# Kernel optimization log

Hardware: AMD Instinct MI355X
Metric: run time of the kernel (lower is better)

Reference implementation:

```python
import jax, jax.numpy as jnp
import numpy as np

N = 100000   # nodes
E = 600000   # edges
D = 128      # in_dim == out_dim
ED = 6       # edge_dim
LN_EPS = 1e-5


def setup_inputs() -> dict:
    key = jax.random.key(0)
    ks = jax.random.split(key, 12)
    s = 1.0 / np.sqrt(D)
    se = 1.0 / np.sqrt(ED)
    return {
        "x": jax.random.normal(ks[0], (N, D), dtype=jnp.float32),
        "edge_index": jax.random.randint(ks[1], (2, E), 0, N, dtype=jnp.int64),
        "edge_attr": jax.random.normal(ks[2], (E, ED), dtype=jnp.float32),
        "batch": jnp.zeros((N,), dtype=jnp.int64),
        "W_e": jax.random.uniform(ks[3], (ED, D), jnp.float32, -se, se),
        "b_e": jax.random.uniform(ks[4], (D,), jnp.float32, -se, se),
        "eps": jnp.zeros((), dtype=jnp.float32),  # GINE train_eps init 0
        "W1": jax.random.uniform(ks[5], (D, D), jnp.float32, -s, s),
        "b1": jax.random.uniform(ks[6], (D,), jnp.float32, -s, s),
        "W2": jax.random.uniform(ks[7], (D, D), jnp.float32, -s, s),
        "b2": jax.random.uniform(ks[8], (D,), jnp.float32, -s, s),
        "gamma": jnp.ones((D,), dtype=jnp.float32),
        "beta": jnp.zeros((D,), dtype=jnp.float32),
    }


def reference(x, edge_index, edge_attr, batch, W_e, b_e, eps, W1, b1, W2, b2, gamma, beta):
    src, dst = edge_index[0], edge_index[1]
    # edge embedding: Linear(edge_dim -> in_dim)
    edge_emb = edge_attr @ W_e + b_e                      # [E, D]
    # GINEConv message: ReLU(x_j + edge_emb), scatter-add to target nodes
    msg = jax.nn.relu(x[src] + edge_emb)                  # [E, D]
    agg = jax.ops.segment_sum(msg, dst, num_segments=N)   # [N, D]
    h = (1.0 + eps) * x + agg                             # [N, D]
    # GINE nn: Linear -> ReLU -> Linear
    h = jax.nn.relu(h @ W1 + b1) @ W2 + b2                # [N, D]
    # LayerNorm over feature dim
    mu = jnp.mean(h, axis=-1, keepdims=True)
    var = jnp.var(h, axis=-1, keepdims=True)
    h = (h - mu) * jax.lax.rsqrt(var + LN_EPS) * gamma + beta
    # activation=True -> ReLU; dropout identity in eval mode
    return jax.nn.relu(h)
```

## Files before the change

kernel.cpp:

```cpp
#include <hip/hip_runtime.h>
#include <stdint.h>

#define NN 100000
#define EE 600000
#define DD 128

typedef _Float16 half8 __attribute__((ext_vector_type(8)));
typedef _Float16 h2 __attribute__((ext_vector_type(2)));
typedef float f32x4 __attribute__((ext_vector_type(4)));

static __device__ __forceinline__ uint32_t pack2(float a, float b) {
    h2 h; h.x = (_Float16)a; h.y = (_Float16)b;
    return __builtin_bit_cast(uint32_t, h);
}
static __device__ __forceinline__ h2 cvt22(float2 f) {
    h2 r; r.x = (_Float16)f.x; r.y = (_Float16)f.y; return r;
}
static __device__ __forceinline__ h2 bc_lo(h2 v) { h2 r; r.x = v.x; r.y = v.x; return r; }
static __device__ __forceinline__ h2 bc_hi(h2 v) { h2 r; r.x = v.y; r.y = v.y; return r; }

static __device__ __forceinline__ void edge_msg(uint32_t rY, uint32_t rZ, uint32_t rW,
                                                uint32_t xv, uint32_t bb,
                                                uint32_t w0, uint32_t w1, uint32_t w2,
                                                uint32_t w3, uint32_t w4, uint32_t w5,
                                                float wgt, float& ax, float& ay)
{
    uint32_t m;
    asm("v_pk_add_f16 %0, %1, %2" : "=v"(m) : "v"(xv), "v"(bb));
    asm("v_pk_fma_f16 %0, %1, %2, %0 op_sel:[0,0,0] op_sel_hi:[0,1,1]" : "+v"(m) : "v"(rY), "v"(w0));
    asm("v_pk_fma_f16 %0, %1, %2, %0 op_sel:[1,0,0] op_sel_hi:[1,1,1]" : "+v"(m) : "v"(rY), "v"(w1));
    asm("v_pk_fma_f16 %0, %1, %2, %0 op_sel:[0,0,0] op_sel_hi:[0,1,1]" : "+v"(m) : "v"(rZ), "v"(w2));
    asm("v_pk_fma_f16 %0, %1, %2, %0 op_sel:[1,0,0] op_sel_hi:[1,1,1]" : "+v"(m) : "v"(rZ), "v"(w3));
    asm("v_pk_fma_f16 %0, %1, %2, %0 op_sel:[0,0,0] op_sel_hi:[0,1,1]" : "+v"(m) : "v"(rW), "v"(w4));
    asm("v_pk_fma_f16 %0, %1, %2, %0 op_sel:[1,0,0] op_sel_hi:[1,1,1]" : "+v"(m) : "v"(rW), "v"(w5));
    asm("v_pk_max_f16 %0, %0, 0" : "+v"(m));
    h2 mh = __builtin_bit_cast(h2, m);
    ax = fmaf(wgt, (float)mh.x, ax);
    ay = fmaf(wgt, (float)mh.y, ay);
}

#define NB_HIST ((EE + 255) / 256)
#define NB_CONV (NN * DD / 4 / 256)
template<bool CONV>
__global__ __launch_bounds__(256)
void setup_kernel(const int* __restrict__ ei, const float* __restrict__ x,
                  const float* __restrict__ W1, const float* __restrict__ W2,
                  int* __restrict__ counts, uint32_t* __restrict__ xh,
                  _Float16* __restrict__ w1h, _Float16* __restrict__ w2h)
{
    const int nbc = CONV ? NB_CONV : 0;
    const int b = blockIdx.x, tid = threadIdx.x;
    if (b < NB_HIST) {
        int e = b * 256 + tid;
        if (e < EE) atomicAdd(&counts[ei[EE + e]], 1);
    } else if (CONV && b < NB_HIST + nbc) {
        int i = (b - NB_HIST) * 256 + tid;
        float4 v = ((const float4*)x)[i];
        uint2 o; o.x = pack2(v.x, v.y); o.y = pack2(v.z, v.w);
        ((uint2*)xh)[i] = o;
    } else {
        int t = (b - NB_HIST - nbc) * 256 + tid;
        if (t < 2 * DD * DD) {
            int which = t >> 14;
            int idx = t & (DD * DD - 1);
            int k = idx >> 7, d = idx & 127;
            float wv = (which ? W2 : W1)[k * DD + d];
            int kt = k >> 5, kr = k & 31;
            int grp = kr >> 3, j = kr & 7;
            int nt = d >> 4, cc = d & 15;
            int off = ((kt * 8 + nt) * 64 + grp * 16 + cc) * 8 + j;
            (which ? w2h : w1h)[off] = (_Float16)wv;
        }
    }
}

__global__ __launch_bounds__(256)
void scan_blocks(const int* __restrict__ counts, int* __restrict__ startv,
                 int* __restrict__ bsum)
{
    const int t = threadIdx.x;
    const int idx = blockIdx.x * 1024 + t * 4;
    int4 v = {0, 0, 0, 0};
    if (idx < NN) v = *(const int4*)(counts + idx);
    int s1 = v.x + v.y, s2 = s1 + v.z, s3 = s2 + v.w;
    const int lane = t & 63;
    int q = s3;
#pragma unroll
    for (int off = 1; off < 64; off <<= 1) {
        int u = __shfl_up(q, off, 64);
        if (lane >= off) q += u;
    }
    __shared__ int wsum[4];
    if (lane == 63) wsum[t >> 6] = q;
    __syncthreads();
    const int w = t >> 6;
    int pre = 0;
    if (w > 0) pre += wsum[0];
    if (w > 1) pre += wsum[1];
    if (w > 2) pre += wsum[2];
    const int excl = (q - s3) + pre;
    if (idx < NN) {
        int4 o = {excl, excl + v.x, excl + s1, excl + s2};
        *(int4*)(startv + idx) = o;
    }
    __syncthreads();
    if (t == 0) bsum[blockIdx.x] = wsum[0] + wsum[1] + wsum[2] + wsum[3];
}

__global__ __launch_bounds__(128)
void scan_top(const int* __restrict__ bsum, int* __restrict__ boff)
{
    __shared__ int sm[128];
    const int t = threadIdx.x;
    const int NB = (NN + 1023) / 1024;
    int v = (t < NB) ? bsum[t] : 0;
    sm[t] = v;
    __syncthreads();
#pragma unroll
    for (int off = 1; off < 128; off <<= 1) {
        int u = (t >= off) ? sm[t - off] : 0;
        __syncthreads();
        sm[t] += u;
        __syncthreads();
    }
    boff[t] = sm[t] - v;
}

__global__ __launch_bounds__(256)
void scatter_rec(const int* __restrict__ ei, const float* __restrict__ ea,
                 const int* __restrict__ start, const int* __restrict__ boff,
                 int* __restrict__ cursor, float* __restrict__ rec)
{
    int e = blockIdx.x * 256 + threadIdx.x;
    if (e >= EE) return;
    int dst = ei[EE + e];
    int src = ei[e];
    int pos = start[dst] + boff[dst >> 10] + atomicAdd(&cursor[dst], 1);
    const float2* eap = (const float2*)(ea + e * 6);
    float2 e01 = eap[0];
    float2 e23 = eap[1];
    float2 e45 = eap[2];
    float4 r;
    r.x = __int_as_float(src);
    r.y = __uint_as_float(pack2(e01.x, e01.y));
    r.z = __uint_as_float(pack2(e23.x, e23.y));
    r.w = __uint_as_float(pack2(e45.x, e45.y));
    *(float4*)(rec + (size_t)pos * 4) = r;
}

#define NWAVE 8192
__global__ __launch_bounds__(256)
void agg_pk2(const float* __restrict__ x, const uint32_t* __restrict__ xh,
             const float* __restrict__ rec, const float* __restrict__ We,
             const float* __restrict__ be, const int* __restrict__ start,
             const int* __restrict__ boff, const int* __restrict__ counts,
             const float* __restrict__ epsp, uint32_t* __restrict__ h0h)
{
    const int w = blockIdx.x * 4 + (threadIdx.x >> 6);
    const int lane = threadIdx.x & 63;
    const int d0 = lane * 2;
    const uint32_t w0u = __builtin_bit_cast(uint32_t, cvt22(*(const float2*)(We + 0 * DD + d0)));
    const uint32_t w1u = __builtin_bit_cast(uint32_t, cvt22(*(const float2*)(We + 1 * DD + d0)));
    const uint32_t w2u = __builtin_bit_cast(uint32_t, cvt22(*(const float2*)(We + 2 * DD + d0)));
    const uint32_t w3u = __builtin_bit_cast(uint32_t, cvt22(*(const float2*)(We + 3 * DD + d0)));
    const uint32_t w4u = __builtin_bit_cast(uint32_t, cvt22(*(const float2*)(We + 4 * DD + d0)));
    const uint32_t w5u = __builtin_bit_cast(uint32_t, cvt22(*(const float2*)(We + 5 * DD + d0)));
    const uint32_t bbu = __builtin_bit_cast(uint32_t, cvt22(*(const float2*)(be + d0)));
    const float sc = 1.0f + epsp[0];
    const int n0 = (int)(((long long)w * NN) >> 13);
    const int n1 = (int)(((long long)(w + 1) * NN) >> 13);

    for (int n = n0; n < n1; ++n) {
        const int begin = start[n] + boff[n >> 10];
        const int cnt = counts[n];
        const float4* rp = (const float4*)rec + begin;
        float ax = 0.f, ay = 0.f;
        for (int i = 0; i < cnt; i += 4) {
            const int rem = cnt - i;
            const int ia = i;
            const int ib = i + (rem > 1 ? 1 : 0);
            const int ic = i + (rem > 2 ? 2 : 0);
            const int id = i + (rem > 3 ? 3 : 0);
            float4 ra = rp[ia], rb = rp[ib], rc = rp[ic], rd = rp[id];
            uint32_t sa = (uint32_t)__float_as_int(ra.x), sb = (uint32_t)__float_as_int(rb.x),
                     sc3 = (uint32_t)__float_as_int(rc.x), sd = (uint32_t)__float_as_int(rd.x);
            uint32_t xa = xh[(sa << 6) + lane];
            uint32_t xb = xh[(sb << 6) + lane];
            uint32_t xc = xh[(sc3 << 6) + lane];
            uint32_t xd = xh[(sd << 6) + lane];
            const float wb = rem > 1 ? 1.f : 0.f;
            const float wc = rem > 2 ? 1.f : 0.f;
            const float wd = rem > 3 ? 1.f : 0.f;
            edge_msg(__float_as_uint(ra.y), __float_as_uint(ra.z), __float_as_uint(ra.w),
                     xa, bbu, w0u, w1u, w2u, w3u, w4u, w5u, 1.f, ax, ay);
            edge_msg(__float_as_uint(rb.y), __float_as_uint(rb.z), __float_as_uint(rb.w),
                     xb, bbu, w0u, w1u, w2u, w3u, w4u, w5u, wb, ax, ay);
            edge_msg(__float_as_uint(rc.y), __float_as_uint(rc.z), __float_as_uint(rc.w),
                     xc, bbu, w0u, w1u, w2u, w3u, w4u, w5u, wc, ax, ay);
            edge_msg(__float_as_uint(rd.y), __float_as_uint(rd.z), __float_as_uint(rd.w),
                     xd, bbu, w0u, w1u, w2u, w3u, w4u, w5u, wd, ax, ay);
        }
        float2 xn = *(const float2*)(x + (size_t)n * DD + d0);
        h0h[(size_t)n * 64 + lane] = pack2(fmaf(sc, xn.x, ax), fmaf(sc, xn.y, ay));
    }
}

__global__ __launch_bounds__(256)
void agg_pk(const float* __restrict__ x, const float* __restrict__ rec,
            const float* __restrict__ We, const float* __restrict__ be,
            const int* __restrict__ start, const int* __restrict__ boff,
            const int* __restrict__ counts, const float* __restrict__ epsp,
            uint32_t* __restrict__ h0h)
{
    const int w = blockIdx.x * 4 + (threadIdx.x >> 6);
    const int lane = threadIdx.x & 63;
    const int d0 = lane * 2;
    const h2 w0h = cvt22(*(const float2*)(We + 0 * DD + d0));
    const h2 w1h = cvt22(*(const float2*)(We + 1 * DD + d0));
    const h2 w2h = cvt22(*(const float2*)(We + 2 * DD + d0));
    const h2 w3h = cvt22(*(const float2*)(We + 3 * DD + d0));
    const h2 w4h = cvt22(*(const float2*)(We + 4 * DD + d0));
    const h2 w5h = cvt22(*(const float2*)(We + 5 * DD + d0));
    const h2 bbh = cvt22(*(const float2*)(be + d0));
    h2 zero2; zero2.x = (_Float16)0.f; zero2.y = (_Float16)0.f;
    const float sc = 1.0f + epsp[0];
    const int n0 = (int)(((long long)w * NN) >> 13);
    const int n1 = (int)(((long long)(w + 1) * NN) >> 13);

    for (int n = n0; n < n1; ++n) {
        const int begin = start[n] + boff[n >> 10];
        const int cnt = counts[n];
        const float4* rp = (const float4*)rec + begin;
        float ax = 0.f, ay = 0.f;
        for (int i = 0; i < cnt; ++i) {
            float4 r = rp[i];
            int s = __float_as_int(r.x);
            h2 c01 = __builtin_bit_cast(h2, r.y);
            h2 c23 = __builtin_bit_cast(h2, r.z);
            h2 c45 = __builtin_bit_cast(h2, r.w);
            h2 emb = bbh;
            emb = bc_lo(c01) * w0h + emb;
            emb = bc_hi(c01) * w1h + emb;
            emb = bc_lo(c23) * w2h + emb;
            emb = bc_hi(c23) * w3h + emb;
            emb = bc_lo(c45) * w4h + emb;
            emb = bc_hi(c45) * w5h + emb;
            h2 m = emb + cvt22(*(const float2*)(x + (size_t)s * DD + d0));
            m = __builtin_elementwise_max(m, zero2);
            ax += (float)m.x;
            ay += (float)m.y;
        }
        float2 xn = *(const float2*)(x + (size_t)n * DD + d0);
        h0h[(size_t)n * 64 + lane] = pack2(fmaf(sc, xn.x, ax), fmaf(sc, xn.y, ay));
    }
}

__global__ __launch_bounds__(256)
void prep_w(const float* __restrict__ W1, const float* __restrict__ W2,
            _Float16* __restrict__ w1h, _Float16* __restrict__ w2h)
{
    int t = blockIdx.x * 256 + threadIdx.x;
    if (t >= 2 * DD * DD) return;
    int which = t >> 14;
    int idx = t & (DD * DD - 1);
    int k = idx >> 7, d = idx & 127;
    float wv = (which ? W2 : W1)[k * DD + d];
    int kt = k >> 5, kr = k & 31;
    int grp = kr >> 3, j = kr & 7;
    int nt = d >> 4, cc = d & 15;
    int off = ((kt * 8 + nt) * 64 + grp * 16 + cc) * 8 + j;
    (which ? w2h : w1h)[off] = (_Float16)wv;
}

__global__ __launch_bounds__(256)
void edge_kernel(const float* __restrict__ x, const int* __restrict__ ei,
                 const float* __restrict__ ea, const float* __restrict__ We,
                 const float* __restrict__ be, float* agg)
{
    int tid = blockIdx.x * 256 + threadIdx.x;
    int d0 = (tid & 31) * 4;
    float4 w0 = *(const float4*)(We + 0 * DD + d0);
    float4 w1 = *(const float4*)(We + 1 * DD + d0);
    float4 w2 = *(const float4*)(We + 2 * DD + d0);
    float4 w3 = *(const float4*)(We + 3 * DD + d0);
    float4 w4 = *(const float4*)(We + 4 * DD + d0);
    float4 w5 = *(const float4*)(We + 5 * DD + d0);
    float4 bb = *(const float4*)(be + d0);
    int estride = (gridDim.x * 256) >> 5;
    for (int e = tid >> 5; e < EE; e += estride) {
        int src = ei[e];
        int dst = ei[EE + e];
        const float2* eap = (const float2*)(ea + e * 6);
        float2 e01 = eap[0];
        float2 e23 = eap[1];
        float2 e45 = eap[2];
        float4 xj = *(const float4*)(x + (size_t)src * DD + d0);
        float mx = xj.x + bb.x + e01.x*w0.x + e01.y*w1.x + e23.x*w2.x + e23.y*w3.x + e45.x*w4.x + e45.y*w5.x;
        float my = xj.y + bb.y + e01.x*w0.y + e01.y*w1.y + e23.x*w2.y + e23.y*w3.y + e45.x*w4.y + e45.y*w5.y;
        float mz = xj.z + bb.z + e01.x*w0.z + e01.y*w1.z + e23.x*w2.z + e23.y*w3.z + e45.x*w4.z + e45.y*w5.z;
        float mw = xj.w + bb.w + e01.x*w0.w + e01.y*w1.w + e23.x*w2.w + e23.y*w3.w + e45.x*w4.w + e45.y*w5.w;
        float* ap = agg + (size_t)dst * DD + d0;
        atomicAdd(ap + 0, fmaxf(mx, 0.f));
        atomicAdd(ap + 1, fmaxf(my, 0.f));
        atomicAdd(ap + 2, fmaxf(mz, 0.f));
        atomicAdd(ap + 3, fmaxf(mw, 0.f));
    }
}

template<int MODE>
__global__ __launch_bounds__(256)
void node2(const void* __restrict__ h0p, const float* __restrict__ xp,
           const _Float16* __restrict__ w1h, const _Float16* __restrict__ w2h,
           const float* __restrict__ b1, const float* __restrict__ b2,
           const float* __restrict__ gamma, const float* __restrict__ beta,
           const float* __restrict__ epsp, float* __restrict__ out)
{
    __shared__ _Float16 h1buf[4][16 * 128];
    const int wv = threadIdx.x >> 6;
    const int l  = threadIdx.x & 63;
    const int lm = l & 15;
    const int lg = l >> 4;
    const int rbase = blockIdx.x * 128 + wv * 32;

    float gam[8], bet[8];
#pragma unroll
    for (int nt = 0; nt < 8; ++nt) {
        gam[nt] = gamma[nt * 16 + lm];
        bet[nt] = beta[nt * 16 + lm];
    }

    for (int t = 0; t < 2; ++t) {
        const int r0 = rbase + t * 16;
        int arow = r0 + lm;
        if (arow >= NN) arow = NN - 1;

        half8 a1[4];
#pragma unroll
        for (int kt = 0; kt < 4; ++kt) {
            const int kb = kt * 32 + lg * 8;
            if constexpr (MODE == 0) {
                a1[kt] = *(const half8*)((const _Float16*)h0p + (size_t)arow * DD + kb);
            } else {
                const float4* hp = (const float4*)((const float*)h0p + (size_t)arow * DD + kb);
                float4 p0 = hp[0], p1 = hp[1];
                const float scale = 1.0f + epsp[0];
                const float4* xr = (const float4*)(xp + (size_t)arow * DD + kb);
                float4 x0 = xr[0], x1 = xr[1];
                float v[8] = { x0.x*scale+p0.x, x0.y*scale+p0.y, x0.z*scale+p0.z, x0.w*scale+p0.w,
                               x1.x*scale+p1.x, x1.y*scale+p1.y, x1.z*scale+p1.z, x1.w*scale+p1.w };
#pragma unroll
                for (int j = 0; j < 8; ++j) a1[kt][j] = (_Float16)v[j];
            }
        }

        f32x4 acc[8];
#pragma unroll
        for (int nt = 0; nt < 8; ++nt) { acc[nt][0]=0.f; acc[nt][1]=0.f; acc[nt][2]=0.f; acc[nt][3]=0.f; }
#pragma unroll
        for (int kt = 0; kt < 4; ++kt) {
#pragma unroll
            for (int nt = 0; nt < 8; ++nt) {
                half8 bh = *(const half8*)(w1h + ((size_t)((kt * 8 + nt) * 64 + l)) * 8);
                acc[nt] = __builtin_amdgcn_mfma_f32_16x16x32_f16(a1[kt], bh, acc[nt], 0, 0, 0);
            }
        }

        _Float16* hb = h1buf[wv];
#pragma unroll
        for (int nt = 0; nt < 8; ++nt) {
            const int col = nt * 16 + lm;
            const float bias = b1[col];
#pragma unroll
            for (int q = 0; q < 4; ++q) {
                const int row = lg * 4 + q;
                float v1 = fmaxf(acc[nt][q] + bias, 0.f);
                hb[row * 128 + (col ^ ((row & 7) << 4))] = (_Float16)v1;
            }
        }

        half8 a2[4];
        {
            const int sw = (lm & 7) << 4;
            const _Float16* rowp = hb + lm * 128;
#pragma unroll
            for (int kt = 0; kt < 4; ++kt) {
                const int kb = kt * 32 + lg * 8;
                a2[kt] = *(const half8*)(rowp + (kb ^ sw));
            }
        }

        f32x4 acc2[8];
#pragma unroll
        for (int nt = 0; nt < 8; ++nt) { acc2[nt][0]=0.f; acc2[nt][1]=0.f; acc2[nt][2]=0.f; acc2[nt][3]=0.f; }
#pragma unroll
        for (int kt = 0; kt < 4; ++kt) {
#pragma unroll
            for (int nt = 0; nt < 8; ++nt) {
                half8 bh = *(const half8*)(w2h + ((size_t)((kt * 8 + nt) * 64 + l)) * 8);
                acc2[nt] = __builtin_amdgcn_mfma_f32_16x16x32_f16(a2[kt], bh, acc2[nt], 0, 0, 0);
            }
        }

        float vv[8][4];
        float sums[4] = {0,0,0,0}, sqs[4] = {0,0,0,0};
#pragma unroll
        for (int nt = 0; nt < 8; ++nt) {
            const int col = nt * 16 + lm;
            const float bias = b2[col];
#pragma unroll
            for (int q = 0; q < 4; ++q) {
                float v2 = acc2[nt][q] + bias;
                vv[nt][q] = v2;
                sums[q] += v2;
                sqs[q]  += v2 * v2;
            }
        }
#pragma unroll
        for (int m = 1; m < 16; m <<= 1) {
#pragma unroll
            for (int q = 0; q < 4; ++q) {
                sums[q] += __shfl_xor(sums[q], m, 64);
                sqs[q]  += __shfl_xor(sqs[q],  m, 64);
            }
        }
#pragma unroll
        for (int q = 0; q < 4; ++q) {
            const int grow = r0 + lg * 4 + q;
            if (grow < NN) {
                const float mu  = sums[q] * (1.f / 128.f);
                const float var = sqs[q] * (1.f / 128.f) - mu * mu;
                const float rs  = rsqrtf(var + 1e-5f);
#pragma unroll
                for (int nt = 0; nt < 8; ++nt) {
                    out[(size_t)grow * DD + nt * 16 + lm] =
                        fmaxf((vv[nt][q] - mu) * rs * gam[nt] + bet[nt], 0.f);
                }
            }
        }
    }
}

extern "C" void kernel_launch(void* const* d_in, const int* in_sizes, int n_in,
                              void* d_out, int out_size, void* d_ws, size_t ws_size,
                              hipStream_t stream) {
    (void)in_sizes; (void)n_in; (void)out_size;
    const float* x     = (const float*)d_in[0];
    const int*   ei    = (const int*)d_in[1];
    const float* ea    = (const float*)d_in[2];
    const float* We    = (const float*)d_in[4];
    const float* be    = (const float*)d_in[5];
    const float* epsp  = (const float*)d_in[6];
    const float* W1    = (const float*)d_in[7];
    const float* b1    = (const float*)d_in[8];
    const float* W2    = (const float*)d_in[9];
    const float* b2    = (const float*)d_in[10];
    const float* gamma = (const float*)d_in[11];
    const float* beta  = (const float*)d_in[12];
    float* out = (float*)d_out;

    char* ws = (char*)d_ws;
    _Float16* w1h = (_Float16*)ws;
    _Float16* w2h = w1h + DD * DD;
    size_t off = 2 * (size_t)DD * DD * sizeof(_Float16);
    int* counts = (int*)(ws + off);   off += (size_t)NN * 4;
    int* cursor = (int*)(ws + off);   off += (size_t)NN * 4;
    int* start  = (int*)(ws + off);   off += (size_t)NN * 4;
    int* bsum   = (int*)(ws + off);   off += 512;
    int* boff   = (int*)(ws + off);   off += 512;
    float* rec  = (float*)(ws + off); off += (size_t)EE * 16;
    uint32_t* h0h = (uint32_t*)(ws + off); off += (size_t)NN * DD * 2;
    const size_t need_h0 = off;
    uint32_t* xh  = (uint32_t*)(ws + off); off += (size_t)NN * DD * 2;
    const size_t need_xh = off;

    const int node_blocks = (NN + 127) / 128;
    const int NBLK = (NN + 1023) / 1024;

    if (ws_size >= need_h0) {
        const bool conv = (ws_size >= need_xh);
        hipMemsetAsync(counts, 0, 2 * (size_t)NN * 4, stream);
        if (conv) {
            setup_kernel<true><<<NB_HIST + NB_CONV + 128, 256, 0, stream>>>(
                ei, x, W1, W2, counts, xh, w1h, w2h);
        } else {
            setup_kernel<false><<<NB_HIST + 128, 256, 0, stream>>>(
                ei, x, W1, W2, counts, xh, w1h, w2h);
        }
        scan_blocks<<<NBLK, 256, 0, stream>>>(counts, start, bsum);
        scan_top<<<1, 128, 0, stream>>>(bsum, boff);
        scatter_rec<<<(EE + 255) / 256, 256, 0, stream>>>(ei, ea, start, boff, cursor, rec);
        if (conv) {
            agg_pk2<<<NWAVE / 4, 256, 0, stream>>>(x, xh, rec, We, be, start, boff,
                                                   counts, epsp, h0h);
        } else {
            agg_pk<<<NWAVE / 4, 256, 0, stream>>>(x, rec, We, be, start, boff,
                                                  counts, epsp, h0h);
        }
        node2<0><<<node_blocks, 256, 0, stream>>>(h0h, x, w1h, w2h, b1, b2,
                                                  gamma, beta, epsp, out);
    } else {
        hipMemsetAsync(d_out, 0, (size_t)NN * DD * sizeof(float), stream);
        prep_w<<<(2 * DD * DD + 255) / 256, 256, 0, stream>>>(W1, W2, w1h, w2h);
        edge_kernel<<<2048, 256, 0, stream>>>(x, ei, ea, We, be, out);
        node2<2><<<node_blocks, 256, 0, stream>>>(out, x, w1h, w2h, b1, b2,
                                                  gamma, beta, epsp, out);
    }
}
```

Before: 177.3 us.

## Stream edges across node boundaries per wave instead of per-node padded loops

The aggregation kernel now walks the contiguous CSR edge range owned by each wave in groups of four, flushing node accumulators whenever an edge crosses a node boundary. Before, each node's edge list was padded up to a multiple of four, with masked duplicate loads. Node start offsets are loaded once per wave into lanes and fetched with shuffles. The edge message also folds the bias into the first FMA and adds x after the edge terms, which drops the weight multiply. This cuts wasted padded gather work and per-node overhead, at the cost of a data-dependent inner while loop and more branching.

```diff
diff --git a/kernel.cpp b/kernel.cpp
--- a/kernel.cpp
+++ b/kernel.cpp
@@ -19,24 +19,22 @@
 static __device__ __forceinline__ h2 bc_lo(h2 v) { h2 r; r.x = v.x; r.y = v.x; return r; }
 static __device__ __forceinline__ h2 bc_hi(h2 v) { h2 r; r.x = v.y; r.y = v.y; return r; }
 
-static __device__ __forceinline__ void edge_msg(uint32_t rY, uint32_t rZ, uint32_t rW,
-                                                uint32_t xv, uint32_t bb,
-                                                uint32_t w0, uint32_t w1, uint32_t w2,
-                                                uint32_t w3, uint32_t w4, uint32_t w5,
-                                                float wgt, float& ax, float& ay)
+static __device__ __forceinline__ uint32_t edge_msg2(uint32_t rY, uint32_t rZ, uint32_t rW,
+                                                     uint32_t xv, uint32_t bb,
+                                                     uint32_t w0, uint32_t w1, uint32_t w2,
+                                                     uint32_t w3, uint32_t w4, uint32_t w5)
 {
     uint32_t m;
-    asm("v_pk_add_f16 %0, %1, %2" : "=v"(m) : "v"(xv), "v"(bb));
-    asm("v_pk_fma_f16 %0, %1, %2, %0 op_sel:[0,0,0] op_sel_hi:[0,1,1]" : "+v"(m) : "v"(rY), "v"(w0));
+    asm("v_pk_fma_f16 %0, %1, %2, %3 op_sel:[0,0,0] op_sel_hi:[0,1,1]"
+        : "=v"(m) : "v"(rY), "v"(w0), "v"(bb));
     asm("v_pk_fma_f16 %0, %1, %2, %0 op_sel:[1,0,0] op_sel_hi:[1,1,1]" : "+v"(m) : "v"(rY), "v"(w1));
     asm("v_pk_fma_f16 %0, %1, %2, %0 op_sel:[0,0,0] op_sel_hi:[0,1,1]" : "+v"(m) : "v"(rZ), "v"(w2));
     asm("v_pk_fma_f16 %0, %1, %2, %0 op_sel:[1,0,0] op_sel_hi:[1,1,1]" : "+v"(m) : "v"(rZ), "v"(w3));
     asm("v_pk_fma_f16 %0, %1, %2, %0 op_sel:[0,0,0] op_sel_hi:[0,1,1]" : "+v"(m) : "v"(rW), "v"(w4));
     asm("v_pk_fma_f16 %0, %1, %2, %0 op_sel:[1,0,0] op_sel_hi:[1,1,1]" : "+v"(m) : "v"(rW), "v"(w5));
+    asm("v_pk_add_f16 %0, %0, %1" : "+v"(m) : "v"(xv));
     asm("v_pk_max_f16 %0, %0, 0" : "+v"(m));
-    h2 mh = __builtin_bit_cast(h2, m);
-    ax = fmaf(wgt, (float)mh.x, ax);
-    ay = fmaf(wgt, (float)mh.y, ay);
+    return m;
 }
 
 #define NB_HIST ((EE + 255) / 256)
@@ -150,11 +148,11 @@
 
 #define NWAVE 8192
 __global__ __launch_bounds__(256)
-void agg_pk2(const float* __restrict__ x, const uint32_t* __restrict__ xh,
-             const float* __restrict__ rec, const float* __restrict__ We,
-             const float* __restrict__ be, const int* __restrict__ start,
-             const int* __restrict__ boff, const int* __restrict__ counts,
-             const float* __restrict__ epsp, uint32_t* __restrict__ h0h)
+void agg_stream(const float* __restrict__ x, const uint32_t* __restrict__ xh,
+                const float4* __restrict__ rec, const float* __restrict__ We,
+                const float* __restrict__ be, const int* __restrict__ start,
+                const int* __restrict__ boff, const float* __restrict__ epsp,
+                uint32_t* __restrict__ h0h)
 {
     const int w = blockIdx.x * 4 + (threadIdx.x >> 6);
     const int lane = threadIdx.x & 63;
@@ -169,39 +167,69 @@
     const float sc = 1.0f + epsp[0];
     const int n0 = (int)(((long long)w * NN) >> 13);
     const int n1 = (int)(((long long)(w + 1) * NN) >> 13);
-
-    for (int n = n0; n < n1; ++n) {
-        const int begin = start[n] + boff[n >> 10];
-        const int cnt = counts[n];
-        const float4* rp = (const float4*)rec + begin;
-        float ax = 0.f, ay = 0.f;
-        for (int i = 0; i < cnt; i += 4) {
-            const int rem = cnt - i;
-            const int ia = i;
-            const int ib = i + (rem > 1 ? 1 : 0);
-            const int ic = i + (rem > 2 ? 2 : 0);
-            const int id = i + (rem > 3 ? 3 : 0);
-            float4 ra = rp[ia], rb = rp[ib], rc = rp[ic], rd = rp[id];
-            uint32_t sa = (uint32_t)__float_as_int(ra.x), sb = (uint32_t)__float_as_int(rb.x),
-                     sc3 = (uint32_t)__float_as_int(rc.x), sd = (uint32_t)__float_as_int(rd.x);
-            uint32_t xa = xh[(sa << 6) + lane];
-            uint32_t xb = xh[(sb << 6) + lane];
-            uint32_t xc = xh[(sc3 << 6) + lane];
-            uint32_t xd = xh[(sd << 6) + lane];
-            const float wb = rem > 1 ? 1.f : 0.f;
-            const float wc = rem > 2 ? 1.f : 0.f;
-            const float wd = rem > 3 ? 1.f : 0.f;
-            edge_msg(__float_as_uint(ra.y), __float_as_uint(ra.z), __float_as_uint(ra.w),
-                     xa, bbu, w0u, w1u, w2u, w3u, w4u, w5u, 1.f, ax, ay);
-            edge_msg(__float_as_uint(rb.y), __float_as_uint(rb.z), __float_as_uint(rb.w),
-                     xb, bbu, w0u, w1u, w2u, w3u, w4u, w5u, wb, ax, ay);
-            edge_msg(__float_as_uint(rc.y), __float_as_uint(rc.z), __float_as_uint(rc.w),
-                     xc, bbu, w0u, w1u, w2u, w3u, w4u, w5u, wc, ax, ay);
-            edge_msg(__float_as_uint(rd.y), __float_as_uint(rd.z), __float_as_uint(rd.w),
-                     xd, bbu, w0u, w1u, w2u, w3u, w4u, w5u, wd, ax, ay);
-        }
-        float2 xn = *(const float2*)(x + (size_t)n * DD + d0);
+    const int span = n1 - n0;
+
+    int gs = 0;
+    {
+        int nidx = n0 + lane;
+        if (lane <= span) {
+            gs = (nidx < NN) ? (start[nidx] + boff[nidx >> 10]) : EE;
+        }
+    }
+    const int ebase = __shfl(gs, 0, 64);
+    const int eend  = __shfl(gs, span, 64);
+
+    int n = n0;
+    int nstop = __shfl(gs, 1, 64);
+    float2 xn = *(const float2*)(x + (size_t)n0 * DD + d0);
+    float ax = 0.f, ay = 0.f;
+
+#define STEP(K, MK)                                                              \
+    {                                                                            \
+        const int ek = e + K;                                                    \
+        if (ek < eend) {                                                         \
+            while (ek >= nstop) {                                                \
+                h0h[(size_t)n * 64 + lane] =                                     \
+                    pack2(fmaf(sc, xn.x, ax), fmaf(sc, xn.y, ay));               \
+                ax = 0.f; ay = 0.f; ++n;                                         \
+                xn = *(const float2*)(x + (size_t)n * DD + d0);                  \
+                nstop = __shfl(gs, n - n0 + 1, 64);                              \
+            }                                                                    \
+            h2 mh = __builtin_bit_cast(h2, MK);                                  \
+            ax += (float)mh.x; ay += (float)mh.y;                                \
+        }                                                                        \
+    }
+
+    for (int e = ebase; e < eend; e += 4) {
+        const int last = eend - 1;
+        const int i0 = e;
+        const int i1 = (e + 1 < eend) ? e + 1 : last;
+        const int i2 = (e + 2 < eend) ? e + 2 : last;
+        const int i3 = (e + 3 < eend) ? e + 3 : last;
+        float4 r0 = rec[i0], r1 = rec[i1], r2 = rec[i2], r3 = rec[i3];
+        uint32_t xa = xh[((uint32_t)__float_as_int(r0.x) << 6) + lane];
+        uint32_t xb = xh[((uint32_t)__float_as_int(r1.x) << 6) + lane];
+        uint32_t xc = xh[((uint32_t)__float_as_int(r2.x) << 6) + lane];
+        uint32_t xd = xh[((uint32_t)__float_as_int(r3.x) << 6) + lane];
+        uint32_t m0 = edge_msg2(__float_as_uint(r0.y), __float_as_uint(r0.z), __float_as_uint(r0.w),
+                                xa, bbu, w0u, w1u, w2u, w3u, w4u, w5u);
+        uint32_t m1 = edge_msg2(__float_as_uint(r1.y), __float_as_uint(r1.z), __float_as_uint(r1.w),
+                                xb, bbu, w0u, w1u, w2u, w3u, w4u, w5u);
+        uint32_t m2 = edge_msg2(__float_as_uint(r2.y), __float_as_uint(r2.z), __float_as_uint(r2.w),
+                                xc, bbu, w0u, w1u, w2u, w3u, w4u, w5u);
+        uint32_t m3 = edge_msg2(__float_as_uint(r3.y), __float_as_uint(r3.z), __float_as_uint(r3.w),
+                                xd, bbu, w0u, w1u, w2u, w3u, w4u, w5u);
+        STEP(0, m0)
+        STEP(1, m1)
+        STEP(2, m2)
+        STEP(3, m3)
+    }
+#undef STEP
+
+    while (n < n1) {
         h0h[(size_t)n * 64 + lane] = pack2(fmaf(sc, xn.x, ax), fmaf(sc, xn.y, ay));
+        ax = 0.f; ay = 0.f; ++n;
+        if (n < n1) xn = *(const float2*)(x + (size_t)n * DD + d0);
     }
 }
 
@@ -490,8 +518,8 @@
         scan_top<<<1, 128, 0, stream>>>(bsum, boff);
         scatter_rec<<<(EE + 255) / 256, 256, 0, stream>>>(ei, ea, start, boff, cursor, rec);
         if (conv) {
-            agg_pk2<<<NWAVE / 4, 256, 0, stream>>>(x, xh, rec, We, be, start, boff,
-                                                   counts, epsp, h0h);
+            agg_stream<<<NWAVE / 4, 256, 0, stream>>>(x, xh, (const float4*)rec, We, be,
+                                                      start, boff, epsp, h0h);
         } else {
             agg_pk<<<NWAVE / 4, 256, 0, stream>>>(x, rec, We, be, start, boff,
                                                   counts, epsp, h0h);
```

After: 158.7 us. -10.5%, faster.
